# Optimization experiments

Hardware: AMD Instinct MI355X
Metric: run time of the kernel (lower is better)

The kernel has to match this reference:

```python
import jax, jax.numpy as jnp
import numpy as np

N_NODES = 50000
N_EDGES = 800000
HID = 256
TDIM = 128


def setup_inputs() -> dict:
    key = jax.random.key(0)
    ks = jax.random.split(key, 16)
    s = 1.0 / np.sqrt(HID)
    inp = {
        "hidden": jax.random.normal(ks[0], (N_NODES, HID), dtype=jnp.float32),
        "t": jax.random.uniform(ks[1], (1,), dtype=jnp.float32) * 100.0,
        "src": jax.random.randint(ks[2], (N_EDGES,), 0, N_NODES, dtype=jnp.int32),
        "dst": jax.random.randint(ks[3], (N_EDGES,), 0, N_NODES, dtype=jnp.int32),
        # GraphConv layer 1 (relu) and layer 2 weights: [in, out]
        "W1": jax.random.normal(ks[4], (HID, HID), dtype=jnp.float32) * s,
        "b1": jnp.zeros((HID,), dtype=jnp.float32),
        "W2": jax.random.normal(ks[5], (HID, HID), dtype=jnp.float32) * s,
        "b2": jnp.zeros((HID,), dtype=jnp.float32),
        # TimeEncode: cos(t * w + b)
        "time_w": jnp.asarray(1.0 / 10.0 ** np.linspace(0, 9, TDIM), dtype=jnp.float32),
        "time_b": jnp.zeros((TDIM,), dtype=jnp.float32),
        # GRUCell params (torch layout: [3*H, in], gate order r,z,n)
        "W_ih": jax.random.normal(ks[6], (3 * HID, HID + TDIM), dtype=jnp.float32) * s,
        "W_hh": jax.random.normal(ks[7], (3 * HID, HID), dtype=jnp.float32) * s,
        "b_ih": jnp.zeros((3 * HID,), dtype=jnp.float32),
        "b_hh": jnp.zeros((3 * HID,), dtype=jnp.float32),
    }
    return inp


def _gcn_layer(x, W, b, src, dst, out_norm, in_norm, relu):
    # DGL GraphConv, norm='both', in==out feats -> aggregate then matmul
    h = x * out_norm[:, None]
    agg = jax.ops.segment_sum(h[src], dst, num_segments=N_NODES)
    agg = agg * in_norm[:, None]
    out = agg @ W + b
    return jax.nn.relu(out) if relu else out


def reference(hidden, t, src, dst, W1, b1, W2, b2, time_w, time_b, W_ih, W_hh, b_ih, b_hh):
    ones = jnp.ones((N_EDGES,), dtype=hidden.dtype)
    outdeg = jax.ops.segment_sum(ones, src, num_segments=N_NODES)
    indeg = jax.ops.segment_sum(ones, dst, num_segments=N_NODES)
    out_norm = jnp.clip(outdeg, 1.0, None) ** -0.5
    in_norm = jnp.clip(indeg, 1.0, None) ** -0.5

    # StackedGCN: k_hop-1 relu layers + final layer (no activation)
    h = _gcn_layer(hidden, W1, b1, src, dst, out_norm, in_norm, relu=True)
    h = _gcn_layer(h, W2, b2, src, dst, out_norm, in_norm, relu=False)
    h = jax.nn.relu(h)

    # time encoding: cos(t * w + b), broadcast to all nodes
    te = jnp.cos(t[0] * time_w + time_b)  # [TDIM]
    te = jnp.broadcast_to(te, (h.shape[0], TDIM))

    x = jnp.concatenate([h, te], axis=1)  # [N, HID+TDIM]

    # GRUCell (torch semantics)
    gi = x @ W_ih.T + b_ih
    gh = h @ W_hh.T + b_hh
    i_r, i_z, i_n = jnp.split(gi, 3, axis=1)
    h_r, h_z, h_n = jnp.split(gh, 3, axis=1)
    r = jax.nn.sigmoid(i_r + h_r)
    z = jax.nn.sigmoid(i_z + h_z)
    n = jnp.tanh(i_n + r * h_n)
    return (1.0 - z) * n + z * h
```

## Files before the change

### kernel.cpp

```cpp
#include <hip/hip_runtime.h>
#include <cstdint>
#include <cstddef>

#define NN 50000
#define NE 800000
#define HID 256
#define TDIM 128

#define CHB 16384
#define NSL 64
#define SLE (NE / NSL)

typedef short bf16x8 __attribute__((ext_vector_type(8)));
typedef float f32x4 __attribute__((ext_vector_type(4)));

#define GLOAD_LDS16(g, l)                                                        \
  __builtin_amdgcn_global_load_lds(                                              \
      (const __attribute__((address_space(1))) unsigned int*)(g),                \
      (__attribute__((address_space(3))) unsigned int*)(l), 16, 0, 0)

__device__ inline unsigned short f2bf(float f) {
  uint32_t u = __builtin_bit_cast(uint32_t, f);
  uint32_t r = u + 0x7FFFu + ((u >> 16) & 1u);
  return (unsigned short)(r >> 16);
}
__device__ inline float bf2f(unsigned short s) {
  uint32_t u = ((uint32_t)s) << 16;
  return __builtin_bit_cast(float, u);
}
__device__ inline float fast_sig(float x) {
  return __builtin_amdgcn_rcpf(1.0f + __expf(-x));
}
__device__ inline float fast_tanh(float x) {
  float xc = fminf(fmaxf(x, -10.0f), 10.0f);
  float e = __expf(2.0f * xc);
  return 1.0f - 2.0f * __builtin_amdgcn_rcpf(e + 1.0f);
}

__global__ __launch_bounds__(1024) void prep_a(const int* __restrict__ src,
                                               const int* __restrict__ dst,
                                               int* __restrict__ P,
                                               const float* __restrict__ x,
                                               short* __restrict__ xb,
                                               unsigned char* __restrict__ xf8) {
  const int b = blockIdx.x;
  if (b < 8 * NSL) {
    __shared__ int h[CHB];
    const int c = b & 7, s = b >> 3;
    for (int j = threadIdx.x; j < CHB; j += 1024) h[j] = 0;
    __syncthreads();
    const int* arr = (c < 4) ? src : dst;
    const int base = (c & 3) * CHB;
    const int e0 = s * SLE;
    for (int i = threadIdx.x; i < SLE; i += 1024) {
      int v = arr[e0 + i] - base;
      if ((unsigned)v < CHB) atomicAdd(&h[v], 1);
    }
    __syncthreads();
    int* Pc = P + (size_t)(c * NSL + s) * CHB;
    for (int j = threadIdx.x; j < CHB; j += 1024) Pc[j] = h[j];
  } else {
    int i = (b - 8 * NSL) * 1024 + threadIdx.x;
    if (i < NN * HID / 4) {
      float4 v = ((const float4*)x)[i];
      unsigned int lo = (unsigned int)f2bf(v.x) | ((unsigned int)f2bf(v.y) << 16);
      unsigned int hi = (unsigned int)f2bf(v.z) | ((unsigned int)f2bf(v.w) << 16);
      ((uint2*)xb)[i] = make_uint2(lo, hi);
      unsigned int f8 = __builtin_amdgcn_cvt_pk_fp8_f32(v.x, v.y, 0u, false);
      f8 = __builtin_amdgcn_cvt_pk_fp8_f32(v.z, v.w, f8, true);
      ((unsigned int*)xf8)[i] = f8;
    }
  }
}

__global__ __launch_bounds__(256) void hist_reduce(int* __restrict__ P,
                                                   float* __restrict__ onorm,
                                                   float* __restrict__ inorm,
                                                   int* __restrict__ icnt) {
  int n = blockIdx.x * 256 + threadIdx.x;
  if (n >= 4 * CHB) return;
  const int c = n >> 14, j = n & (CHB - 1);
  int* Po = P + (size_t)(c * NSL) * CHB + j;
  int od = 0;
#pragma unroll 8
  for (int s = 0; s < NSL; ++s) od += Po[(size_t)s * CHB];
  int* Pi = P + (size_t)((4 + c) * NSL) * CHB + j;
  int run = 0;
#pragma unroll 8
  for (int s = 0; s < NSL; ++s) { int t = Pi[(size_t)s * CHB]; Pi[(size_t)s * CHB] = run; run += t; }
  if (n < NN) {
    onorm[n] = 1.0f / sqrtf(fmaxf((float)od, 1.0f));
    inorm[n] = 1.0f / sqrtf(fmaxf((float)run, 1.0f));
    icnt[n] = run;
  }
}

__global__ __launch_bounds__(1024) void scan_rows(const int* __restrict__ icnt,
                                                  int* __restrict__ rowstart) {
  __shared__ int wsum[16];
  __shared__ int carry_s;
  const int tid = threadIdx.x, lane = tid & 63, w = tid >> 6;
  if (tid == 0) { carry_s = 0; rowstart[0] = 0; }
  __syncthreads();
  for (int base = 0; base < NN; base += 8192) {
    int i0 = base + tid * 8;
    int c[8];
    int v = 0;
#pragma unroll
    for (int j = 0; j < 8; ++j) {
      int i = i0 + j;
      c[j] = (i < NN) ? icnt[i] : 0;
      v += c[j];
    }
    int inc = v;
#pragma unroll
    for (int off = 1; off < 64; off <<= 1) {
      int t = __shfl_up(inc, off, 64);
      if (lane >= off) inc += t;
    }
    if (lane == 63) wsum[w] = inc;
    __syncthreads();
    int woff = 0;
    for (int k = 0; k < w; ++k) woff += wsum[k];
    int carry = carry_s;
    int run = carry + woff + inc - v;
#pragma unroll
    for (int j = 0; j < 8; ++j) {
      int i = i0 + j;
      if (i < NN) rowstart[i + 1] = run + c[j];
      run += c[j];
    }
    __syncthreads();
    if (tid == 1023) carry_s = carry + woff + inc;
    __syncthreads();
  }
}

__global__ __launch_bounds__(1024) void fill_csr2(const int* __restrict__ src,
                                                  const int* __restrict__ dst,
                                                  const float* __restrict__ onorm,
                                                  const int* __restrict__ rowstart,
                                                  const int* __restrict__ P,
                                                  uint2* __restrict__ epk) {
  __shared__ int cur[CHB];
  const int b = blockIdx.x;
  const int c = b & 3, s = b >> 2;
  const int base = c * CHB;
  const int* Pi = P + (size_t)((4 + c) * NSL + s) * CHB;
  for (int j = threadIdx.x; j < CHB; j += 1024) {
    int n = base + j;
    cur[j] = (n < NN ? rowstart[n] : 0) + Pi[j];
  }
  __syncthreads();
  const int e0 = s * SLE;
  for (int i = threadIdx.x; i < SLE; i += 1024) {
    int d = dst[e0 + i] - base;
    if ((unsigned)d < CHB) {
      int sv = src[e0 + i];
      int pos = atomicAdd(&cur[d], 1);
      epk[pos] = make_uint2((unsigned)sv, __builtin_bit_cast(unsigned, onorm[sv]));
    }
  }
}

__global__ __launch_bounds__(256) void gather_agg(const unsigned char* __restrict__ xF8,
                                                  const int* __restrict__ rowstart,
                                                  const uint2* __restrict__ epk,
                                                  const float* __restrict__ inorm,
                                                  short* __restrict__ aggB) {
  const int wid = blockIdx.x * 4 + (threadIdx.x >> 6);
  const int l = threadIdx.x & 63;
  if (wid >= NN) return;
  const int half = l >> 5;
  const int fo2 = (l & 31) * 8;
  const int e1 = rowstart[wid + 1];
  int e = rowstart[wid];
  float a[8] = {0.f, 0.f, 0.f, 0.f, 0.f, 0.f, 0.f, 0.f};

  for (; e + 8 <= e1; e += 8) {
    uint2 pe[4]; uint2 uu[4];
#pragma unroll
    for (int q = 0; q < 4; ++q) pe[q] = epk[e + q * 2 + half];
#pragma unroll
    for (int q = 0; q < 4; ++q) uu[q] = *(const uint2*)(xF8 + (size_t)pe[q].x * HID + fo2);
#pragma unroll
    for (int q = 0; q < 4; ++q) {
      float wq = __builtin_bit_cast(float, pe[q].y);
      a[0] = fmaf(__builtin_amdgcn_cvt_f32_fp8(uu[q].x, 0), wq, a[0]);
      a[1] = fmaf(__builtin_amdgcn_cvt_f32_fp8(uu[q].x, 1), wq, a[1]);
      a[2] = fmaf(__builtin_amdgcn_cvt_f32_fp8(uu[q].x, 2), wq, a[2]);
      a[3] = fmaf(__builtin_amdgcn_cvt_f32_fp8(uu[q].x, 3), wq, a[3]);
      a[4] = fmaf(__builtin_amdgcn_cvt_f32_fp8(uu[q].y, 0), wq, a[4]);
      a[5] = fmaf(__builtin_amdgcn_cvt_f32_fp8(uu[q].y, 1), wq, a[5]);
      a[6] = fmaf(__builtin_amdgcn_cvt_f32_fp8(uu[q].y, 2), wq, a[6]);
      a[7] = fmaf(__builtin_amdgcn_cvt_f32_fp8(uu[q].y, 3), wq, a[7]);
    }
  }
  for (; e < e1; e += 2) {
    int idx = e + half;
    bool v = idx < e1;
    uint2 pe = v ? epk[idx] : make_uint2(0u, 0u);
    float w0 = v ? __builtin_bit_cast(float, pe.y) : 0.0f;
    uint2 u = *(const uint2*)(xF8 + (size_t)pe.x * HID + fo2);
    a[0] = fmaf(__builtin_amdgcn_cvt_f32_fp8(u.x, 0), w0, a[0]);
    a[1] = fmaf(__builtin_amdgcn_cvt_f32_fp8(u.x, 1), w0, a[1]);
    a[2] = fmaf(__builtin_amdgcn_cvt_f32_fp8(u.x, 2), w0, a[2]);
    a[3] = fmaf(__builtin_amdgcn_cvt_f32_fp8(u.x, 3), w0, a[3]);
    a[4] = fmaf(__builtin_amdgcn_cvt_f32_fp8(u.y, 0), w0, a[4]);
    a[5] = fmaf(__builtin_amdgcn_cvt_f32_fp8(u.y, 1), w0, a[5]);
    a[6] = fmaf(__builtin_amdgcn_cvt_f32_fp8(u.y, 2), w0, a[6]);
    a[7] = fmaf(__builtin_amdgcn_cvt_f32_fp8(u.y, 3), w0, a[7]);
  }

#pragma unroll
  for (int k = 0; k < 8; ++k) a[k] += __shfl_xor(a[k], 32);

  if (l < 32) {
    const float wi = inorm[wid];
    uint4 o;
    o.x = (unsigned int)f2bf(a[0] * wi) | ((unsigned int)f2bf(a[1] * wi) << 16);
    o.y = (unsigned int)f2bf(a[2] * wi) | ((unsigned int)f2bf(a[3] * wi) << 16);
    o.z = (unsigned int)f2bf(a[4] * wi) | ((unsigned int)f2bf(a[5] * wi) << 16);
    o.w = (unsigned int)f2bf(a[6] * wi) | ((unsigned int)f2bf(a[7] * wi) << 16);
    *(uint4*)(aggB + (size_t)wid * HID + fo2) = o;
  }
}

__global__ __launch_bounds__(256) void wprep(const float* __restrict__ W1,
                                             const float* __restrict__ W2,
                                             const float* __restrict__ W_ih,
                                             const float* __restrict__ W_hh,
                                             const float* __restrict__ t,
                                             const float* __restrict__ tw,
                                             const float* __restrict__ tb,
                                             const float* __restrict__ b_ih,
                                             const float* __restrict__ b_hh,
                                             short* __restrict__ W1B,
                                             short* __restrict__ W2B,
                                             short* __restrict__ WgB,
                                             float* __restrict__ cst) {
  const int b = blockIdx.x;
  const int k = threadIdx.x;
  if (b < 256) {
    W1B[b * 256 + k] = (short)f2bf(W1[k * 256 + b]);
    W2B[b * 256 + k] = (short)f2bf(W2[k * 256 + b]);
  } else if (b < 512) {
    int u = b - 256;
    int base = (u >> 4) * 64 + (u & 15);
    float v0 = W_ih[(size_t)u * 384 + k] + W_hh[(size_t)u * 256 + k];
    float v1 = W_ih[(size_t)(256 + u) * 384 + k] + W_hh[(size_t)(256 + u) * 256 + k];
    float v2 = W_ih[(size_t)(512 + u) * 384 + k];
    float v3 = W_hh[(size_t)(512 + u) * 256 + k];
    WgB[(size_t)(base + 0)  * 256 + k] = (short)f2bf(v0);
    WgB[(size_t)(base + 16) * 256 + k] = (short)f2bf(v1);
    WgB[(size_t)(base + 32) * 256 + k] = (short)f2bf(v2);
    WgB[(size_t)(base + 48) * 256 + k] = (short)f2bf(v3);
  } else {
    __shared__ float te[TDIM];
    int u = k;
    if (u < TDIM) te[u] = cosf(t[0] * tw[u] + tb[u]);
    __syncthreads();
    float cr = b_ih[u] + b_hh[u];
    float cz = b_ih[256 + u] + b_hh[256 + u];
    float ci = b_ih[512 + u];
    for (int kk = 0; kk < TDIM; ++kk) {
      float tk = te[kk];
      cr = fmaf(tk, W_ih[(size_t)u * 384 + 256 + kk], cr);
      cz = fmaf(tk, W_ih[(size_t)(256 + u) * 384 + 256 + kk], cz);
      ci = fmaf(tk, W_ih[(size_t)(512 + u) * 384 + 256 + kk], ci);
    }
    cst[u] = cr;
    cst[256 + u] = cz;
    cst[512 + u] = ci;
    cst[768 + u] = b_hh[512 + u];
  }
}

template <int NP, bool GRUE, bool BF16O, bool F8O>
__global__ __launch_bounds__(256, 3) void panel_gemm(const short* __restrict__ A,
                                                     const short* __restrict__ WB,
                                                     const float* __restrict__ bias,
                                                     const float* __restrict__ cst,
                                                     short* __restrict__ outH,
                                                     unsigned char* __restrict__ outF8,
                                                     float* __restrict__ outF) {
  __shared__ __align__(16) short Ps[64 * 256];

  const int row0 = blockIdx.x * 64;
  const int tid = threadIdx.x;
  const int l = tid & 63, w = tid >> 6;
  const int fr = l & 15, fg = l >> 4;

#pragma unroll
  for (int i = 0; i < 8; ++i) {
    int id = tid + i * 256;
    int row = id >> 5, kc = id & 31;
    GLOAD_LDS16(WB + (size_t)row * HID + ((kc ^ (row & 15)) << 3), Ps + id * 8);
  }

  int ar = row0 + w * 16 + fr;
  ar = ar < NN ? ar : NN - 1;
  bf16x8 af[8];
#pragma unroll
  for (int t = 0; t < 8; ++t)
    af[t] = *(const bf16x8*)(A + (size_t)ar * HID + t * 32 + fg * 8);

  __syncthreads();

#pragma unroll
  for (int p = 0; p < NP; ++p) {
    f32x4 acc[4];
    acc[0] = acc[1] = acc[2] = acc[3] = (f32x4)(0.0f);
#pragma unroll
    for (int t = 0; t < 8; ++t) {
#pragma unroll
      for (int nf = 0; nf < 4; ++nf) {
        int rr = nf * 16 + fr;
        bf16x8 bh = *(const bf16x8*)(Ps + rr * 256 + (((t * 4 + fg) ^ (rr & 15)) << 3));
        acc[nf] = __builtin_amdgcn_mfma_f32_16x16x32_bf16(af[t], bh, acc[nf], 0, 0, 0);
      }
    }

    if constexpr (!GRUE) {
#pragma unroll
      for (int nf = 0; nf < 4; ++nf) {
        int c = p * 64 + nf * 16 + fr;
        float bs = bias[c];
#pragma unroll
        for (int j = 0; j < 4; ++j) {
          int row = row0 + w * 16 + fg * 4 + j;
          if (row < NN) {
            float v = fmaxf(acc[nf][j] + bs, 0.0f);
            size_t off = (size_t)row * HID + c;
            if constexpr (BF16O) outH[off] = (short)f2bf(v);
            if constexpr (F8O) {
              unsigned int r8 = __builtin_amdgcn_cvt_pk_fp8_f32(v, v, 0u, false);
              outF8[off] = (unsigned char)(r8 & 0xFF);
            }
          }
        }
      }
    } else {
      const int u = p * 16 + fr;
      const float cr = cst[u], cz = cst[256 + u], ci = cst[512 + u], chn = cst[768 + u];
#pragma unroll
      for (int j = 0; j < 4; ++j) {
        int row = row0 + w * 16 + fg * 4 + j;
        if (row < NN) {
          float dr = acc[0][j] + cr;
          float dz = acc[1][j] + cz;
          float dn = acc[2][j] + ci;
          float dh = acc[3][j] + chn;
          float rg = fast_sig(dr);
          float zg = fast_sig(dz);
          float ng = fast_tanh(dn + rg * dh);
          size_t off = (size_t)row * HID + u;
          float hv = bf2f((unsigned short)A[off]);
          outF[off] = (1.0f - zg) * ng + zg * hv;
        }
      }
    }

    if (p + 1 < NP) {
      __syncthreads();
#pragma unroll
      for (int i = 0; i < 8; ++i) {
        int id = tid + i * 256;
        int row = id >> 5, kc = id & 31;
        GLOAD_LDS16(WB + (size_t)((p + 1) * 64 + row) * HID + ((kc ^ (row & 15)) << 3),
                    Ps + id * 8);
      }
      __syncthreads();
    }
  }
}

extern "C" void kernel_launch(void* const* d_in, const int* in_sizes, int n_in,
                              void* d_out, int out_size, void* d_ws, size_t ws_size,
                              hipStream_t stream) {
  const float* hidden = (const float*)d_in[0];
  const float* t      = (const float*)d_in[1];
  const int*   src    = (const int*)d_in[2];
  const int*   dst    = (const int*)d_in[3];
  const float* W1     = (const float*)d_in[4];
  const float* b1     = (const float*)d_in[5];
  const float* W2     = (const float*)d_in[6];
  const float* b2     = (const float*)d_in[7];
  const float* time_w = (const float*)d_in[8];
  const float* time_b = (const float*)d_in[9];
  const float* W_ih   = (const float*)d_in[10];
  const float* W_hh   = (const float*)d_in[11];
  const float* b_ih   = (const float*)d_in[12];
  const float* b_hh   = (const float*)d_in[13];
  float* out = (float*)d_out;

  char* p = (char*)d_ws;
  float* onorm = (float*)p;      p += 50048 * 4;
  float* inorm = (float*)p;      p += 50048 * 4;
  float* cst   = (float*)p;      p += 1024 * 4;
  int* rowstart = (int*)p;       p += 50052 * 4;
  int* icnt     = (int*)p;       p += 50048 * 4;
  uint2* epk    = (uint2*)p;     p += 800000 * 8;
  const size_t NFE = (size_t)NN * HID;
  short* Xb   = (short*)p;       p += NFE * 2;
  short* aggB = (short*)p;       p += NFE * 2;
  short* h1B  = (short*)p;       p += NFE * 2;
  short* h2B  = (short*)p;       p += NFE * 2;
  unsigned char* Xf8  = (unsigned char*)p;  p += NFE;
  unsigned char* h1F8 = (unsigned char*)p;  p += NFE;
  short* W1B  = (short*)p;       p += 65536 * 2;
  short* W2B  = (short*)p;       p += 65536 * 2;
  short* WgB  = (short*)p;       p += 262144 * 2;
  int* P = (int*)h1B;

  const int cvt_blocks = (NN * HID / 4 + 1023) / 1024;
  prep_a<<<8 * NSL + cvt_blocks, 1024, 0, stream>>>(src, dst, P, hidden, Xb, Xf8);
  wprep<<<513, 256, 0, stream>>>(W1, W2, W_ih, W_hh, t, time_w, time_b, b_ih, b_hh,
                                 W1B, W2B, WgB, cst);

  hist_reduce<<<(4 * CHB + 255) / 256, 256, 0, stream>>>(P, onorm, inorm, icnt);
  scan_rows<<<1, 1024, 0, stream>>>(icnt, rowstart);
  fill_csr2<<<4 * NSL, 1024, 0, stream>>>(src, dst, onorm, rowstart, P, epk);

  const int gather_blocks = (NN + 3) / 4;
  const int gblocks = (NN + 63) / 64;

  gather_agg<<<gather_blocks, 256, 0, stream>>>(Xf8, rowstart, epk, inorm, aggB);
  panel_gemm<4, false, false, true><<<gblocks, 256, 0, stream>>>(aggB, W1B, b1, nullptr, nullptr, h1F8, nullptr);

  gather_agg<<<gather_blocks, 256, 0, stream>>>(h1F8, rowstart, epk, inorm, aggB);
  panel_gemm<4, false, true, false><<<gblocks, 256, 0, stream>>>(aggB, W2B, b2, nullptr, h2B, nullptr, nullptr);

  panel_gemm<16, true, false, false><<<gblocks, 256, 0, stream>>>(h2B, WgB, nullptr, cst, nullptr, nullptr, out);
}
```

Before: 268.5 us.

## Split panel GEMM column panels across two wave groups with double panel buffers

The panel GEMM block grows from 4 to 8 waves. Waves are split by parity so that two 64-column weight panels are computed at once, each from its own LDS buffer, and both panels are loaded together between iterations. This halves the number of serial panel iterations and barrier pairs per block and adds more waves to hide latency. In exchange each block uses twice the LDS (64KB) and loads its A fragments redundantly in both wave groups, which may limit how many blocks fit on a CU.

```diff
diff --git a/kernel.cpp b/kernel.cpp
--- a/kernel.cpp
+++ b/kernel.cpp
@@ -277,28 +277,32 @@
 }
 
 template <int NP, bool GRUE, bool BF16O, bool F8O>
-__global__ __launch_bounds__(256, 3) void panel_gemm(const short* __restrict__ A,
+__global__ __launch_bounds__(512, 4) void panel_gemm(const short* __restrict__ A,
                                                      const short* __restrict__ WB,
                                                      const float* __restrict__ bias,
                                                      const float* __restrict__ cst,
                                                      short* __restrict__ outH,
                                                      unsigned char* __restrict__ outF8,
                                                      float* __restrict__ outF) {
-  __shared__ __align__(16) short Ps[64 * 256];
+  __shared__ __align__(16) short Ps[2][64 * 256];
 
   const int row0 = blockIdx.x * 64;
   const int tid = threadIdx.x;
-  const int l = tid & 63, w = tid >> 6;
+  const int l = tid & 63, wv = tid >> 6;
+  const int rowgrp = wv & 3, parity = wv >> 2;
   const int fr = l & 15, fg = l >> 4;
 
 #pragma unroll
   for (int i = 0; i < 8; ++i) {
-    int id = tid + i * 256;
-    int row = id >> 5, kc = id & 31;
-    GLOAD_LDS16(WB + (size_t)row * HID + ((kc ^ (row & 15)) << 3), Ps + id * 8);
-  }
-
-  int ar = row0 + w * 16 + fr;
+    int id = tid + i * 512;
+    int pp = id >> 11;
+    int cid = id & 2047;
+    int row = cid >> 5, kc = cid & 31;
+    GLOAD_LDS16(WB + (size_t)(pp * 64 + row) * HID + ((kc ^ (row & 15)) << 3),
+                Ps[pp] + cid * 8);
+  }
+
+  int ar = row0 + rowgrp * 16 + fr;
   ar = ar < NN ? ar : NN - 1;
   bf16x8 af[8];
 #pragma unroll
@@ -308,7 +312,8 @@
   __syncthreads();
 
 #pragma unroll
-  for (int p = 0; p < NP; ++p) {
+  for (int r = 0; r < NP / 2; ++r) {
+    const int p = 2 * r + parity;
     f32x4 acc[4];
     acc[0] = acc[1] = acc[2] = acc[3] = (f32x4)(0.0f);
 #pragma unroll
@@ -316,7 +321,7 @@
 #pragma unroll
       for (int nf = 0; nf < 4; ++nf) {
         int rr = nf * 16 + fr;
-        bf16x8 bh = *(const bf16x8*)(Ps + rr * 256 + (((t * 4 + fg) ^ (rr & 15)) << 3));
+        bf16x8 bh = *(const bf16x8*)(Ps[parity] + rr * 256 + (((t * 4 + fg) ^ (rr & 15)) << 3));
         acc[nf] = __builtin_amdgcn_mfma_f32_16x16x32_bf16(af[t], bh, acc[nf], 0, 0, 0);
       }
     }
@@ -328,7 +333,7 @@
         float bs = bias[c];
 #pragma unroll
         for (int j = 0; j < 4; ++j) {
-          int row = row0 + w * 16 + fg * 4 + j;
+          int row = row0 + rowgrp * 16 + fg * 4 + j;
           if (row < NN) {
             float v = fmaxf(acc[nf][j] + bs, 0.0f);
             size_t off = (size_t)row * HID + c;
@@ -345,7 +350,7 @@
       const float cr = cst[u], cz = cst[256 + u], ci = cst[512 + u], chn = cst[768 + u];
 #pragma unroll
       for (int j = 0; j < 4; ++j) {
-        int row = row0 + w * 16 + fg * 4 + j;
+        int row = row0 + rowgrp * 16 + fg * 4 + j;
         if (row < NN) {
           float dr = acc[0][j] + cr;
           float dz = acc[1][j] + cz;
@@ -361,14 +366,16 @@
       }
     }
 
-    if (p + 1 < NP) {
+    if (r + 1 < NP / 2) {
       __syncthreads();
 #pragma unroll
       for (int i = 0; i < 8; ++i) {
-        int id = tid + i * 256;
-        int row = id >> 5, kc = id & 31;
-        GLOAD_LDS16(WB + (size_t)((p + 1) * 64 + row) * HID + ((kc ^ (row & 15)) << 3),
-                    Ps + id * 8);
+        int id = tid + i * 512;
+        int pp = id >> 11;
+        int cid = id & 2047;
+        int row = cid >> 5, kc = cid & 31;
+        GLOAD_LDS16(WB + (size_t)((2 * (r + 1) + pp) * 64 + row) * HID + ((kc ^ (row & 15)) << 3),
+                    Ps[pp] + cid * 8);
       }
       __syncthreads();
     }
@@ -426,10 +433,10 @@
   const int gblocks = (NN + 63) / 64;
 
   gather_agg<<<gather_blocks, 256, 0, stream>>>(Xf8, rowstart, epk, inorm, aggB);
-  panel_gemm<4, false, false, true><<<gblocks, 256, 0, stream>>>(aggB, W1B, b1, nullptr, nullptr, h1F8, nullptr);
+  panel_gemm<4, false, false, true><<<gblocks, 512, 0, stream>>>(aggB, W1B, b1, nullptr, nullptr, h1F8, nullptr);
 
   gather_agg<<<gather_blocks, 256, 0, stream>>>(h1F8, rowstart, epk, inorm, aggB);
-  panel_gemm<4, false, true, false><<<gblocks, 256, 0, stream>>>(aggB, W2B, b2, nullptr, h2B, nullptr, nullptr);
-
-  panel_gemm<16, true, false, false><<<gblocks, 256, 0, stream>>>(h2B, WgB, nullptr, cst, nullptr, nullptr, out);
-}
+  panel_gemm<4, false, true, false><<<gblocks, 512, 0, stream>>>(aggB, W2B, b2, nullptr, h2B, nullptr, nullptr);
+
+  panel_gemm<16, true, false, false><<<gblocks, 512, 0, stream>>>(h2B, WgB, nullptr, cst, nullptr, nullptr, out);
+}
```

Result: slower. 285.3 us (+6.3%).
